# Kernel optimization log

Measured on AMD Instinct MI355X. Metric: run time of the kernel, lower is better.

Reference implementation:

```python
import jax, jax.numpy as jnp
import numpy as np

DIM, HEADS, DHEAD, CTX_DIM = 1024, 16, 64, 768
INNER = HEADS * DHEAD  # 1024
FF_HID = 4 * DIM       # 4096
EPS = 1e-5


def _ln(x, g, b):
    mu = jnp.mean(x, axis=-1, keepdims=True)
    var = jnp.mean(jnp.square(x - mu), axis=-1, keepdims=True)
    return (x - mu) * jax.lax.rsqrt(var + EPS) * g + b


def _attn(x, ctx, Wq, Wk, Wv, Wo, bo):
    b, n, _ = x.shape
    m = ctx.shape[1]
    q = (x @ Wq).reshape(b, n, HEADS, DHEAD)
    k = (ctx @ Wk).reshape(b, m, HEADS, DHEAD)
    v = (ctx @ Wv).reshape(b, m, HEADS, DHEAD)
    scale = DHEAD ** -0.5
    sim = jnp.einsum('bihd,bjhd->bhij', q, k) * scale
    attn = jax.nn.softmax(sim, axis=-1)
    out = jnp.einsum('bhij,bjhd->bihd', attn, v).reshape(b, n, INNER)
    return out @ Wo + bo


def setup_inputs() -> dict:
    key = jax.random.key(0)
    ks = jax.random.split(key, 24)
    def w(k, shape, fan_in):
        return jax.random.normal(k, shape, jnp.float32) * (fan_in ** -0.5)
    inp = {
        'x': jax.random.normal(ks[0], (2, 2048, DIM), jnp.float32),
        'context': jax.random.normal(ks[1], (2, 77, CTX_DIM), jnp.float32),
        # attn1 (self)
        'Wq1': w(ks[2], (DIM, INNER), DIM), 'Wk1': w(ks[3], (DIM, INNER), DIM),
        'Wv1': w(ks[4], (DIM, INNER), DIM), 'Wo1': w(ks[5], (INNER, DIM), INNER),
        'bo1': jnp.zeros((DIM,), jnp.float32),
        # attn2 (cross)
        'Wq2': w(ks[6], (DIM, INNER), DIM), 'Wk2': w(ks[7], (CTX_DIM, INNER), CTX_DIM),
        'Wv2': w(ks[8], (CTX_DIM, INNER), CTX_DIM), 'Wo2': w(ks[9], (INNER, DIM), INNER),
        'bo2': jnp.zeros((DIM,), jnp.float32),
        # GEGLU FFN
        'Wp': w(ks[10], (DIM, 2 * FF_HID), DIM), 'bp': jnp.zeros((2 * FF_HID,), jnp.float32),
        'W2': w(ks[11], (FF_HID, DIM), FF_HID), 'b2': jnp.zeros((DIM,), jnp.float32),
        # LayerNorms
        'g1': jnp.ones((DIM,), jnp.float32), 'be1': jnp.zeros((DIM,), jnp.float32),
        'g2': jnp.ones((DIM,), jnp.float32), 'be2': jnp.zeros((DIM,), jnp.float32),
        'g3': jnp.ones((DIM,), jnp.float32), 'be3': jnp.zeros((DIM,), jnp.float32),
    }
    return inp


def reference(x, context, Wq1, Wk1, Wv1, Wo1, bo1, Wq2, Wk2, Wv2, Wo2, bo2,
              Wp, bp, W2, b2, g1, be1, g2, be2, g3, be3):
    h = _ln(x, g1, be1)
    x = _attn(h, h, Wq1, Wk1, Wv1, Wo1, bo1) + x
    h = _ln(x, g2, be2)
    x = _attn(h, context, Wq2, Wk2, Wv2, Wo2, bo2) + x
    h = _ln(x, g3, be3)
    y = h @ Wp + bp
    a, gate = y[..., :FF_HID], y[..., FF_HID:]
    x = (a * jax.nn.gelu(gate, approximate=False)) @ W2 + b2 + x
    return x
```

## Files before the change

### kernel.cpp

```cpp
#include <hip/hip_runtime.h>
#include <hip/hip_bf16.h>
#include <math.h>

#define DIMN   1024
#define HEADS  16
#define DHEAD  64
#define CTXD   768
#define FFH    4096
#define NTOK   4096
#define SEQ    2048
#define NCTX   77
#define CTOK   154

typedef unsigned short u16;
typedef __bf16 bf16x8 __attribute__((ext_vector_type(8)));
typedef float  f32x4  __attribute__((ext_vector_type(4)));

__device__ __forceinline__ u16 f2bf(float f) {
  union { float f; unsigned u; } c; c.f = f;
  unsigned r = c.u + 0x7FFFu + ((c.u >> 16) & 1u);
  return (u16)(r >> 16);
}
__device__ __forceinline__ float bf2f(u16 h) {
  union { unsigned u; float f; } c; c.u = ((unsigned)h) << 16; return c.f;
}

__device__ __forceinline__ void gload16(const void* g, void* l) {
  __builtin_amdgcn_global_load_lds(
      (__attribute__((address_space(1))) void*)(void*)(g),
      (__attribute__((address_space(3))) void*)(l), 16, 0, 0);
}

__device__ __forceinline__ f32x4 mfma16(bf16x8 a, bf16x8 b, f32x4 c) {
  return __builtin_amdgcn_mfma_f32_16x16x32_bf16(a, b, c, 0, 0, 0);
}

struct WBatch { const float* s[6]; u16* d[6]; };

template<int NB>
__global__ __launch_bounds__(256)
void wconvB_k(WBatch wb, int K, int N)
{
  __shared__ u16 t[64][65];
  const float* __restrict__ W  = wb.s[blockIdx.z];
  u16* __restrict__       WT   = wb.d[blockIdx.z];
  int n0 = blockIdx.x * 64, k0 = blockIdx.y * 64;
  int tid = threadIdx.x;
  int rr = tid >> 4, cc = tid & 15;
#pragma unroll
  for (int i = 0; i < 4; ++i) {
    int kr = rr + i * 16;
    const float4 v = *(const float4*)&W[(size_t)(k0 + kr) * N + n0 + cc * 4];
    t[kr][cc*4+0] = f2bf(v.x); t[kr][cc*4+1] = f2bf(v.y);
    t[kr][cc*4+2] = f2bf(v.z); t[kr][cc*4+3] = f2bf(v.w);
  }
  __syncthreads();
#pragma unroll
  for (int i = 0; i < 4; ++i) {
    int nr = rr + i * 16;
    int r0 = cc * 4;
    ushort4 o;
    o.x = t[r0+0][nr]; o.y = t[r0+1][nr]; o.z = t[r0+2][nr]; o.w = t[r0+3][nr];
    *(ushort4*)&WT[(size_t)(n0 + nr) * K + k0 + r0] = o;
  }
}

__global__ __launch_bounds__(256)
void wconv_k(const float* __restrict__ W, u16* __restrict__ WT, int K, int N)
{
  __shared__ u16 t[64][65];
  int n0 = blockIdx.x * 64, k0 = blockIdx.y * 64;
  int tid = threadIdx.x;
  int rr = tid >> 4, cc = tid & 15;
#pragma unroll
  for (int i = 0; i < 4; ++i) {
    int kr = rr + i * 16;
    const float4 v = *(const float4*)&W[(size_t)(k0 + kr) * N + n0 + cc * 4];
    t[kr][cc*4+0] = f2bf(v.x); t[kr][cc*4+1] = f2bf(v.y);
    t[kr][cc*4+2] = f2bf(v.z); t[kr][cc*4+3] = f2bf(v.w);
  }
  __syncthreads();
#pragma unroll
  for (int i = 0; i < 4; ++i) {
    int nr = rr + i * 16;
    int r0 = cc * 4;
    ushort4 o;
    o.x = t[r0+0][nr]; o.y = t[r0+1][nr]; o.z = t[r0+2][nr]; o.w = t[r0+3][nr];
    *(ushort4*)&WT[(size_t)(n0 + nr) * K + k0 + r0] = o;
  }
}

__global__ void cconv_k(const float* __restrict__ c, u16* __restrict__ o, int n)
{
  int i = blockIdx.x * 256 + threadIdx.x;
  if (i < n) o[i] = f2bf(c[i]);
}

__global__ __launch_bounds__(256)
void ln_k(const float* __restrict__ x, const float* __restrict__ gm,
          const float* __restrict__ bt, u16* __restrict__ o)
{
  int row = blockIdx.x;
  int tid = threadIdx.x;
  const float4 v = *(const float4*)&x[(size_t)row * DIMN + tid * 4];
  float s = v.x + v.y + v.z + v.w;
  float q = v.x*v.x + v.y*v.y + v.z*v.z + v.w*v.w;
#pragma unroll
  for (int off = 32; off; off >>= 1) { s += __shfl_xor(s, off); q += __shfl_xor(q, off); }
  __shared__ float ss[4], qq[4];
  int wave = tid >> 6;
  if ((tid & 63) == 0) { ss[wave] = s; qq[wave] = q; }
  __syncthreads();
  s = ss[0] + ss[1] + ss[2] + ss[3];
  q = qq[0] + qq[1] + qq[2] + qq[3];
  float mu = s * (1.0f / DIMN);
  float var = q * (1.0f / DIMN) - mu * mu;
  float rs = rsqrtf(var + 1e-5f);
  const float4 gv = *(const float4*)&gm[tid * 4];
  const float4 bv = *(const float4*)&bt[tid * 4];
  ushort4 r;
  r.x = f2bf((v.x - mu) * rs * gv.x + bv.x);
  r.y = f2bf((v.y - mu) * rs * gv.y + bv.y);
  r.z = f2bf((v.z - mu) * rs * gv.z + bv.z);
  r.w = f2bf((v.w - mu) * rs * gv.w + bv.w);
  *(ushort4*)&o[(size_t)row * DIMN + tid * 4] = r;
}

__global__ __launch_bounds__(256)
void ln_b_k(const u16* __restrict__ x, const float* __restrict__ gm,
            const float* __restrict__ bt, u16* __restrict__ o)
{
  int row = blockIdx.x;
  int tid = threadIdx.x;
  const ushort4 u = *(const ushort4*)&x[(size_t)row * DIMN + tid * 4];
  float4 v;
  v.x = bf2f(u.x); v.y = bf2f(u.y); v.z = bf2f(u.z); v.w = bf2f(u.w);
  float s = v.x + v.y + v.z + v.w;
  float q = v.x*v.x + v.y*v.y + v.z*v.z + v.w*v.w;
#pragma unroll
  for (int off = 32; off; off >>= 1) { s += __shfl_xor(s, off); q += __shfl_xor(q, off); }
  __shared__ float ss[4], qq[4];
  int wave = tid >> 6;
  if ((tid & 63) == 0) { ss[wave] = s; qq[wave] = q; }
  __syncthreads();
  s = ss[0] + ss[1] + ss[2] + ss[3];
  q = qq[0] + qq[1] + qq[2] + qq[3];
  float mu = s * (1.0f / DIMN);
  float var = q * (1.0f / DIMN) - mu * mu;
  float rs = rsqrtf(var + 1e-5f);
  const float4 gv = *(const float4*)&gm[tid * 4];
  const float4 bv = *(const float4*)&bt[tid * 4];
  ushort4 r;
  r.x = f2bf((v.x - mu) * rs * gv.x + bv.x);
  r.y = f2bf((v.y - mu) * rs * gv.y + bv.y);
  r.z = f2bf((v.z - mu) * rs * gv.z + bv.z);
  r.w = f2bf((v.w - mu) * rs * gv.w + bv.w);
  *(ushort4*)&o[(size_t)row * DIMN + tid * 4] = r;
}

template<int MODE>
__global__ __launch_bounds__(512, 4)
void gemm_k(const u16* __restrict__ A, const u16* __restrict__ Bt,
            int M, int N, int K,
            const float* __restrict__ bias, const float* __restrict__ resid,
            u16* __restrict__ obf, float* __restrict__ of32,
            int seq, int vstride,
            u16* __restrict__ ob2, u16* __restrict__ ob3)
{
  __shared__ __align__(16) u16 As[2][128 * 32];
  __shared__ __align__(16) u16 Bs[2][128 * 32];
  const int tid = threadIdx.x;
  const int lane = tid & 63, wave = tid >> 6;
  const int wr = wave >> 1, wc = wave & 1;
  const int g = lane >> 4, r16 = lane & 15;
  const int m0 = blockIdx.x * 128, n0 = blockIdx.y * 128;

  f32x4 acc[2][4] = {};

  const int srow = tid >> 2;
  const int sch  = tid & 3;
  const int schs = sch ^ ((srow >> 1) & 3);
  const int arow = (m0 + srow > M - 1) ? (M - 1) : (m0 + srow);
  const size_t abase = (size_t)arow * K + schs * 8;
  const size_t bbase = (size_t)(n0 + srow) * K + schs * 8;

  auto stage = [&](int buf, int kt) {
    gload16(A  + abase + kt, &As[buf][tid * 8]);
    gload16(Bt + bbase + kt, &Bs[buf][tid * 8]);
  };

  stage(0, 0);

  const int nkt = K >> 5;
  for (int t = 0; t < nkt; ++t) {
    const int cur = t & 1;
    if (t + 1 < nkt) {
      stage(cur ^ 1, (t + 1) << 5);
      asm volatile("s_waitcnt vmcnt(2)" ::: "memory");
    } else {
      asm volatile("s_waitcnt vmcnt(0)" ::: "memory");
    }
    __builtin_amdgcn_s_barrier();

    bf16x8 af[2], bfr[4];
#pragma unroll
    for (int mi = 0; mi < 2; ++mi) {
      int r = wr * 32 + mi * 16 + r16;
      int cph = g ^ ((r >> 1) & 3);
      af[mi] = *(const bf16x8*)&As[cur][(r * 4 + cph) * 8];
    }
#pragma unroll
    for (int ni = 0; ni < 4; ++ni) {
      int r = wc * 64 + ni * 16 + r16;
      int cph = g ^ ((r >> 1) & 3);
      bfr[ni] = *(const bf16x8*)&Bs[cur][(r * 4 + cph) * 8];
    }
    __builtin_amdgcn_s_setprio(1);
#pragma unroll
    for (int mi = 0; mi < 2; ++mi)
#pragma unroll
      for (int ni = 0; ni < 4; ++ni)
        acc[mi][ni] = mfma16(af[mi], bfr[ni], acc[mi][ni]);
    __builtin_amdgcn_s_setprio(0);

    __builtin_amdgcn_s_barrier();
  }

  const int grp = n0 >> 10;
#pragma unroll
  for (int ni = 0; ni < 4; ++ni) {
    int col = n0 + wc * 64 + ni * 16 + r16;
    float bv = 0.0f;
    if constexpr (MODE == 0) bv = bias ? bias[col] : 0.0f;
    const int c1 = col & 1023;
#pragma unroll
    for (int mi = 0; mi < 2; ++mi) {
      f32x4 c = acc[mi][ni];
#pragma unroll
      for (int rg = 0; rg < 4; ++rg) {
        int row = m0 + wr * 32 + mi * 16 + g * 4 + rg;
        if (row < M) {
          float v = c[rg] + bv;
          if constexpr (MODE == 0) {
            obf[(size_t)row * N + col] = f2bf(v);
          } else if constexpr (MODE == 4) {
            if (grp == 0) {
              obf[(size_t)row * 1024 + c1] = f2bf(v);
            } else if (grp == 1) {
              ob2[(size_t)row * 1024 + c1] = f2bf(v);
            } else {
              int b = row / seq, srow_ = row - b * seq;
              int jg = srow_ >> 6, j = srow_ & 63;
              int pos = jg * 64 + ((j & 15) << 2) + (j >> 4);
              ob3[((size_t)b * HEADS * DHEAD + c1) * vstride + pos] = f2bf(v);
            }
          } else {
            if (grp == 0) {
              obf[(size_t)row * 1024 + c1] = f2bf(v);
            } else {
              int b = row / seq, srow_ = row - b * seq;
              int jg = srow_ >> 6, j = srow_ & 63;
              int pos = jg * 64 + ((j & 15) << 2) + (j >> 4);
              ob3[((size_t)b * HEADS * DHEAD + c1) * vstride + pos] = f2bf(v);
            }
          }
        }
      }
    }
  }
}

template<int MODE>
__global__ __launch_bounds__(512, 2)
void gemm64_k(const u16* __restrict__ A, const u16* __restrict__ Bt,
              int M, int N, int K,
              const float* __restrict__ bias, const float* __restrict__ residf,
              const u16* __restrict__ residb,
              u16* __restrict__ obf, float* __restrict__ of32)
{
  __shared__ __align__(16) u16 As[2][128 * 64];
  __shared__ __align__(16) u16 Bs[2][128 * 64];
  const int tid = threadIdx.x;
  const int lane = tid & 63, wave = tid >> 6;
  const int wr = wave >> 1, wc = wave & 1;
  const int g = lane >> 4, r16 = lane & 15;
  const int m0 = blockIdx.x * 128, n0 = blockIdx.y * 128;

  f32x4 acc[2][4] = {};

  int aro[2], bro[2], scs[2];
#pragma unroll
  for (int i = 0; i < 2; ++i) {
    const int c = tid + i * 512;
    const int r = c >> 3, ch = c & 7;
    scs[i] = ch ^ (r & 7);
    aro[i] = (m0 + r > M - 1) ? (M - 1) : (m0 + r);
    bro[i] = n0 + r;
  }

  auto stage = [&](int buf, int kt) {
#pragma unroll
    for (int i = 0; i < 2; ++i) {
      const int c = tid + i * 512;
      gload16(A  + (size_t)aro[i] * K + kt + scs[i] * 8, &As[buf][c * 8]);
      gload16(Bt + (size_t)bro[i] * K + kt + scs[i] * 8, &Bs[buf][c * 8]);
    }
  };

  stage(0, 0);

  const int nkt = K >> 6;
  for (int t = 0; t < nkt; ++t) {
    const int cur = t & 1;
    if (t + 1 < nkt) {
      stage(cur ^ 1, (t + 1) << 6);
      asm volatile("s_waitcnt vmcnt(4)" ::: "memory");
    } else {
      asm volatile("s_waitcnt vmcnt(0)" ::: "memory");
    }
    __builtin_amdgcn_s_barrier();

#pragma unroll
    for (int ks = 0; ks < 2; ++ks) {
      bf16x8 af[2], bfr[4];
#pragma unroll
      for (int mi = 0; mi < 2; ++mi) {
        int r = wr * 32 + mi * 16 + r16;
        int cph = (ks * 4 + g) ^ (r & 7);
        af[mi] = *(const bf16x8*)&As[cur][(r * 8 + cph) * 8];
      }
#pragma unroll
      for (int ni = 0; ni < 4; ++ni) {
        int r = wc * 64 + ni * 16 + r16;
        int cph = (ks * 4 + g) ^ (r & 7);
        bfr[ni] = *(const bf16x8*)&Bs[cur][(r * 8 + cph) * 8];
      }
      __builtin_amdgcn_s_setprio(1);
#pragma unroll
      for (int mi = 0; mi < 2; ++mi)
#pragma unroll
        for (int ni = 0; ni < 4; ++ni)
          acc[mi][ni] = mfma16(af[mi], bfr[ni], acc[mi][ni]);
      __builtin_amdgcn_s_setprio(0);
    }

    __builtin_amdgcn_s_barrier();
  }

#pragma unroll
  for (int ni = 0; ni < 4; ++ni) {
    int col = n0 + wc * 64 + ni * 16 + r16;
    float bv = bias ? bias[col] : 0.0f;
#pragma unroll
    for (int mi = 0; mi < 2; ++mi) {
      f32x4 c = acc[mi][ni];
#pragma unroll
      for (int rg = 0; rg < 4; ++rg) {
        int row = m0 + wr * 32 + mi * 16 + g * 4 + rg;
        if (row < M) {
          float v = c[rg] + bv;
          size_t o = (size_t)row * N + col;
          if constexpr (MODE == 0) {
            obf[o] = f2bf(v);
          } else if constexpr (MODE == 6) {
            obf[o] = f2bf(v + residf[o]);
          } else if constexpr (MODE == 7) {
            obf[o] = f2bf(v + bf2f(residb[o]));
          } else {
            of32[o] = v + bf2f(residb[o]);
          }
        }
      }
    }
  }
}

__global__ __launch_bounds__(512, 2)
void geglu_k(const u16* __restrict__ A, const u16* __restrict__ B1t,
             const u16* __restrict__ B2t,
             const float* __restrict__ ba, const float* __restrict__ bg,
             u16* __restrict__ out, int M, int N)
{
  __shared__ __align__(16) u16 As[2][128 * 32];
  __shared__ __align__(16) u16 B1s[2][128 * 32];
  __shared__ __align__(16) u16 B2s[2][128 * 32];
  const int tid = threadIdx.x;
  const int lane = tid & 63, wave = tid >> 6;
  const int wr = wave >> 1, wc = wave & 1;
  const int g = lane >> 4, r16 = lane & 15;
  const int m0 = blockIdx.x * 128, n0 = blockIdx.y * 128;
  const int K = 1024;

  f32x4 acca[2][4] = {}, accg[2][4] = {};

  const int srow = tid >> 2;
  const int sch  = tid & 3;
  const int schs = sch ^ ((srow >> 1) & 3);
  const size_t abase = (size_t)(m0 + srow) * K + schs * 8;
  const size_t bbase = (size_t)(n0 + srow) * K + schs * 8;

  auto stage = [&](int buf, int kt) {
    gload16(A   + abase + kt, &As[buf][tid * 8]);
    gload16(B1t + bbase + kt, &B1s[buf][tid * 8]);
    gload16(B2t + bbase + kt, &B2s[buf][tid * 8]);
  };

  stage(0, 0);

  const int nkt = K >> 5;
  for (int t = 0; t < nkt; ++t) {
    const int cur = t & 1;
    if (t + 1 < nkt) {
      stage(cur ^ 1, (t + 1) << 5);
      asm volatile("s_waitcnt vmcnt(3)" ::: "memory");
    } else {
      asm volatile("s_waitcnt vmcnt(0)" ::: "memory");
    }
    __builtin_amdgcn_s_barrier();

    bf16x8 af[2], b1f[4], b2f[4];
#pragma unroll
    for (int mi = 0; mi < 2; ++mi) {
      int r = wr * 32 + mi * 16 + r16;
      int cph = g ^ ((r >> 1) & 3);
      af[mi] = *(const bf16x8*)&As[cur][(r * 4 + cph) * 8];
    }
#pragma unroll
    for (int ni = 0; ni < 4; ++ni) {
      int r = wc * 64 + ni * 16 + r16;
      int cph = g ^ ((r >> 1) & 3);
      b1f[ni] = *(const bf16x8*)&B1s[cur][(r * 4 + cph) * 8];
      b2f[ni] = *(const bf16x8*)&B2s[cur][(r * 4 + cph) * 8];
    }
    __builtin_amdgcn_s_setprio(1);
#pragma unroll
    for (int mi = 0; mi < 2; ++mi)
#pragma unroll
      for (int ni = 0; ni < 4; ++ni) {
        acca[mi][ni] = mfma16(af[mi], b1f[ni], acca[mi][ni]);
        accg[mi][ni] = mfma16(af[mi], b2f[ni], accg[mi][ni]);
      }
    __builtin_amdgcn_s_setprio(0);

    __builtin_amdgcn_s_barrier();
  }

#pragma unroll
  for (int ni = 0; ni < 4; ++ni) {
    int col = n0 + wc * 64 + ni * 16 + r16;
    float bva = ba[col], bvg = bg[col];
#pragma unroll
    for (int mi = 0; mi < 2; ++mi) {
#pragma unroll
      for (int rg = 0; rg < 4; ++rg) {
        int row = m0 + wr * 32 + mi * 16 + g * 4 + rg;
        float a  = acca[mi][ni][rg] + bva;
        float gt = accg[mi][ni][rg] + bvg;
        float gl = 0.5f * gt * (1.0f + erff(gt * 0.70710678f));
        out[(size_t)row * N + col] = f2bf(a * gl);
      }
    }
  }
}

__global__ __launch_bounds__(256)
void attn_k(const u16* __restrict__ q, const u16* __restrict__ k,
            const u16* __restrict__ vt, u16* __restrict__ o,
            int kvlen, int seqk, int vstride)
{
  __shared__ __align__(16) u16 Ks[2][64 * 64];
  __shared__ __align__(16) u16 Vs[2][64 * 64];
  __shared__ __align__(16) u16 Ps[4][32 * 72];
  const int tid = threadIdx.x, lane = tid & 63, wave = tid >> 6;
  const int g = lane >> 4, r16 = lane & 15;

  const int L  = blockIdx.y * 16 + blockIdx.x;
  const int c8 = L & 7, tt = L >> 3;
  const int bx = tt & 15;
  const int bh = c8 + 8 * (tt >> 4);

  const int b = bh >> 4, h = bh & 15;
  const int q0 = bx * 128 + wave * 32;
  const float C = 0.18033688f;

  bf16x8 aq[2][2];
#pragma unroll
  for (int qs = 0; qs < 2; ++qs) {
    const size_t qoff = (size_t)(b * SEQ + q0 + qs * 16 + r16) * DIMN + h * DHEAD;
#pragma unroll
    for (int kc = 0; kc < 2; ++kc)
      aq[qs][kc] = *(const bf16x8*)&q[qoff + kc * 32 + g * 8];
  }
  asm volatile("" :: "v"(aq[0][0]), "v"(aq[0][1]), "v"(aq[1][0]), "v"(aq[1][1]));

  f32x4 oacc[2][4] = {};
  float mi[2][4], li[2][4];
#pragma unroll
  for (int qs = 0; qs < 2; ++qs)
#pragma unroll
    for (int rg = 0; rg < 4; ++rg) { mi[qs][rg] = -3e38f; li[qs][rg] = 0.f; }

  const size_t vtbase = (size_t)(b * HEADS + h) * DHEAD * vstride;
  const size_t kbase  = (size_t)b * seqk * DIMN + h * DHEAD;
  const int nkv = (kvlen + 63) >> 6;

  auto stage = [&](int buf, int kv0) {
#pragma unroll
    for (int i = 0; i < 2; ++i) {
      const int c = tid + i * 256;
      const int row = c >> 3, ch = c & 7;
      const int chs = ch ^ (row & 7);
      int kr = kv0 + row; if (kr > kvlen - 1) kr = kvlen - 1;
      gload16(k + kbase + (size_t)kr * DIMN + chs * 8, &Ks[buf][c * 8]);
    }
#pragma unroll
    for (int i = 0; i < 2; ++i) {
      const int c = tid + i * 256;
      const int row = c >> 3, ch = c & 7;
      const int chs = ch ^ (row & 7);
      gload16(vt + vtbase + (size_t)row * vstride + kv0 + chs * 8, &Vs[buf][c * 8]);
    }
  };

  stage(0, 0);

  for (int kvb = 0; kvb < nkv; ++kvb) {
    const int kv0 = kvb * 64;
    const int cur = kvb & 1;
    if (kvb + 1 < nkv) {
      stage(cur ^ 1, kv0 + 64);
      asm volatile("s_waitcnt vmcnt(4)" ::: "memory");
    } else {
      asm volatile("s_waitcnt vmcnt(0)" ::: "memory");
    }
    __builtin_amdgcn_s_barrier();

    f32x4 sa[2][4];
#pragma unroll
    for (int qs = 0; qs < 2; ++qs)
#pragma unroll
      for (int st = 0; st < 4; ++st) sa[qs][st] = (f32x4){0.f, 0.f, 0.f, 0.f};
    __builtin_amdgcn_s_setprio(1);
#pragma unroll
    for (int st = 0; st < 4; ++st) {
      const int kvr = st * 16 + r16;
#pragma unroll
      for (int kc = 0; kc < 2; ++kc) {
        const int chs = (kc * 4 + g) ^ (kvr & 7);
        const bf16x8 kf = *(const bf16x8*)&Ks[cur][kvr * 64 + chs * 8];
        sa[0][st] = mfma16(aq[0][kc], kf, sa[0][st]);
        sa[1][st] = mfma16(aq[1][kc], kf, sa[1][st]);
      }
    }
    __builtin_amdgcn_s_setprio(0);

    if (kv0 + 64 > kvlen) {
#pragma unroll
      for (int st = 0; st < 4; ++st)
        if (kv0 + st * 16 + r16 >= kvlen) {
#pragma unroll
          for (int qs = 0; qs < 2; ++qs)
#pragma unroll
            for (int rg = 0; rg < 4; ++rg) sa[qs][st][rg] = -3e38f;
        }
    }

    float bad = 0.f;
    float m4v[2][4];
#pragma unroll
    for (int qs = 0; qs < 2; ++qs)
#pragma unroll
      for (int rg = 0; rg < 4; ++rg) {
        float m4 = fmaxf(fmaxf(sa[qs][0][rg], sa[qs][1][rg]),
                         fmaxf(sa[qs][2][rg], sa[qs][3][rg]));
        m4v[qs][rg] = m4;
        bad = fmaxf(bad, m4 - mi[qs][rg]);
      }
    if (__any(bad > 16.0f)) {
#pragma unroll
      for (int qs = 0; qs < 2; ++qs)
#pragma unroll
        for (int rg = 0; rg < 4; ++rg) {
          float mx = m4v[qs][rg];
#pragma unroll
          for (int off = 1; off < 16; off <<= 1) mx = fmaxf(mx, __shfl_xor(mx, off));
          const float nm = fmaxf(mi[qs][rg], mx);
          const float corr = __builtin_amdgcn_exp2f((mi[qs][rg] - nm) * C);
          mi[qs][rg] = nm;
          li[qs][rg] *= corr;
#pragma unroll
          for (int ds = 0; ds < 4; ++ds) oacc[qs][ds][rg] *= corr;
        }
    }

#pragma unroll
    for (int qs = 0; qs < 2; ++qs) {
#pragma unroll
      for (int rg = 0; rg < 4; ++rg) {
        const float mc = mi[qs][rg] * C;
        const float p0 = __builtin_amdgcn_exp2f(__builtin_fmaf(sa[qs][0][rg], C, -mc));
        const float p1 = __builtin_amdgcn_exp2f(__builtin_fmaf(sa[qs][1][rg], C, -mc));
        const float p2 = __builtin_amdgcn_exp2f(__builtin_fmaf(sa[qs][2][rg], C, -mc));
        const float p3 = __builtin_amdgcn_exp2f(__builtin_fmaf(sa[qs][3][rg], C, -mc));
        li[qs][rg] += (p0 + p1) + (p2 + p3);
        unsigned lo, hi;
        asm("v_cvt_pk_bf16_f32 %0, %1, %2" : "=v"(lo) : "v"(p0), "v"(p1));
        asm("v_cvt_pk_bf16_f32 %0, %1, %2" : "=v"(hi) : "v"(p2), "v"(p3));
        const int prow = qs * 16 + g * 4 + rg;
        uint2 pk; pk.x = lo; pk.y = hi;
        *(uint2*)&Ps[wave][prow * 72 + r16 * 4] = pk;
      }
    }

    __builtin_amdgcn_s_setprio(1);
#pragma unroll
    for (int kc = 0; kc < 2; ++kc) {
      const bf16x8 pa0 = *(const bf16x8*)&Ps[wave][(r16)      * 72 + kc * 32 + g * 8];
      const bf16x8 pa1 = *(const bf16x8*)&Ps[wave][(16 + r16) * 72 + kc * 32 + g * 8];
#pragma unroll
      for (int ds = 0; ds < 4; ++ds) {
        const int dr = ds * 16 + r16;
        const int chs = (kc * 4 + g) ^ (dr & 7);
        const bf16x8 vf = *(const bf16x8*)&Vs[cur][dr * 64 + chs * 8];
        oacc[0][ds] = mfma16(pa0, vf, oacc[0][ds]);
        oacc[1][ds] = mfma16(pa1, vf, oacc[1][ds]);
      }
    }
    __builtin_amdgcn_s_setprio(0);

    __builtin_amdgcn_s_barrier();
  }

#pragma unroll
  for (int qs = 0; qs < 2; ++qs)
#pragma unroll
    for (int rg = 0; rg < 4; ++rg) {
      float s = li[qs][rg];
#pragma unroll
      for (int off = 1; off < 16; off <<= 1) s += __shfl_xor(s, off);
      li[qs][rg] = s;
    }

#pragma unroll
  for (int qs = 0; qs < 2; ++qs)
#pragma unroll
    for (int rg = 0; rg < 4; ++rg) {
      const float inv = 1.0f / li[qs][rg];
      const int row = q0 + qs * 16 + g * 4 + rg;
      const size_t base = (size_t)(b * SEQ + row) * DIMN + h * DHEAD;
#pragma unroll
      for (int ds = 0; ds < 4; ++ds)
        o[base + ds * 16 + r16] = f2bf(oacc[qs][ds][rg] * inv);
    }
}

extern "C" void kernel_launch(void* const* d_in, const int* in_sizes, int n_in,
                              void* d_out, int out_size, void* d_ws, size_t ws_size,
                              hipStream_t stream)
{
  const float* x   = (const float*)d_in[0];
  const float* ctx = (const float*)d_in[1];
  const float* Wq1 = (const float*)d_in[2];
  const float* Wk1 = (const float*)d_in[3];
  const float* Wv1 = (const float*)d_in[4];
  const float* Wo1 = (const float*)d_in[5];
  const float* bo1 = (const float*)d_in[6];
  const float* Wq2 = (const float*)d_in[7];
  const float* Wk2 = (const float*)d_in[8];
  const float* Wv2 = (const float*)d_in[9];
  const float* Wo2 = (const float*)d_in[10];
  const float* bo2 = (const float*)d_in[11];
  const float* Wp  = (const float*)d_in[12];
  const float* bp  = (const float*)d_in[13];
  const float* W2  = (const float*)d_in[14];
  const float* b2  = (const float*)d_in[15];
  const float* g1  = (const float*)d_in[16];
  const float* be1 = (const float*)d_in[17];
  const float* g2  = (const float*)d_in[18];
  const float* be2 = (const float*)d_in[19];
  const float* g3  = (const float*)d_in[20];
  const float* be3 = (const float*)d_in[21];

  char* ws = (char*)d_ws;
  size_t off = 0;
  auto alloc = [&](size_t bytes) -> void* {
    void* p = ws + off;
    off += (bytes + 255) & ~(size_t)255;
    return p;
  };

  u16* WqT1 = (u16*)alloc((size_t)1024 * 1024 * 2);
  u16* WkT1 = (u16*)alloc((size_t)1024 * 1024 * 2);
  u16* WvT1 = (u16*)alloc((size_t)1024 * 1024 * 2);
  u16* WoT1 = (u16*)alloc((size_t)1024 * 1024 * 2);
  u16* WqT2 = (u16*)alloc((size_t)1024 * 1024 * 2);
  u16* WkT2 = (u16*)alloc((size_t)1024 * 768 * 2);
  u16* WvT2 = (u16*)alloc((size_t)1024 * 768 * 2);
  u16* WoT2 = (u16*)alloc((size_t)1024 * 1024 * 2);
  u16* WpT  = (u16*)alloc((size_t)8192 * 1024 * 2);
  u16* W2T  = (u16*)alloc((size_t)1024 * 4096 * 2);
  u16* x1b  = (u16*)alloc((size_t)NTOK * DIMN * 2);
  u16* x2b  = (u16*)alloc((size_t)NTOK * DIMN * 2);
  u16* ctxb = (u16*)alloc((size_t)CTOK * CTXD * 2);
  u16* k2b  = (u16*)alloc((size_t)CTOK * DIMN * 2);
  u16* vt2b = (u16*)alloc((size_t)2 * HEADS * DHEAD * 128 * 2);
  u16* hb   = (u16*)alloc((size_t)NTOK * DIMN * 2);
  u16* qb   = (u16*)alloc((size_t)NTOK * DIMN * 2);
  u16* kb   = (u16*)alloc((size_t)NTOK * DIMN * 2);
  u16* vtb  = (u16*)alloc((size_t)NTOK * DIMN * 2);
  u16* ab   = (u16*)alloc((size_t)NTOK * DIMN * 2);
  u16* ub   = qb;

  dim3 blk(256);
  dim3 blk5(512);

  WBatch wb6;
  wb6.s[0] = Wq1; wb6.d[0] = WqT1;
  wb6.s[1] = Wk1; wb6.d[1] = WkT1;
  wb6.s[2] = Wv1; wb6.d[2] = WvT1;
  wb6.s[3] = Wo1; wb6.d[3] = WoT1;
  wb6.s[4] = Wq2; wb6.d[4] = WqT2;
  wb6.s[5] = Wo2; wb6.d[5] = WoT2;
  wconvB_k<6><<<dim3(16, 16, 6), blk, 0, stream>>>(wb6, 1024, 1024);
  WBatch wb2;
  wb2.s[0] = Wk2; wb2.d[0] = WkT2;
  wb2.s[1] = Wv2; wb2.d[1] = WvT2;
  wb2.s[2] = nullptr; wb2.d[2] = nullptr;
  wb2.s[3] = nullptr; wb2.d[3] = nullptr;
  wb2.s[4] = nullptr; wb2.d[4] = nullptr;
  wb2.s[5] = nullptr; wb2.d[5] = nullptr;
  wconvB_k<2><<<dim3(16, 12, 2), blk, 0, stream>>>(wb2, 768, 1024);
  wconv_k<<<dim3(128, 16), blk, 0, stream>>>(Wp, WpT, 1024, 8192);
  wconv_k<<<dim3(16, 64), blk, 0, stream>>>(W2, W2T, 4096, 1024);
  cconv_k<<<dim3((CTOK * CTXD + 255) / 256), blk, 0, stream>>>(ctx, ctxb, CTOK * CTXD);

  ln_k<<<NTOK, 256, 0, stream>>>(x, g1, be1, hb);
  gemm_k<4><<<dim3(32, 24), blk5, 0, stream>>>(hb, WqT1, NTOK, 3072, 1024, nullptr, nullptr, qb, nullptr, SEQ, SEQ, kb, vtb);
  attn_k<<<dim3(16, 32), blk, 0, stream>>>(qb, kb, vtb, ab, SEQ, SEQ, SEQ);
  gemm64_k<6><<<dim3(32, 8), blk5, 0, stream>>>(ab, WoT1, NTOK, 1024, 1024, bo1, x, nullptr, x1b, nullptr);

  ln_b_k<<<NTOK, 256, 0, stream>>>(x1b, g2, be2, hb);
  gemm64_k<0><<<dim3(32, 8), blk5, 0, stream>>>(hb, WqT2, NTOK, 1024, 1024, nullptr, nullptr, nullptr, qb, nullptr);
  gemm_k<5><<<dim3(2, 16), blk5, 0, stream>>>(ctxb, WkT2, CTOK, 2048, 768, nullptr, nullptr, k2b, nullptr, NCTX, 128, nullptr, vt2b);
  attn_k<<<dim3(16, 32), blk, 0, stream>>>(qb, k2b, vt2b, ab, NCTX, NCTX, 128);
  gemm64_k<7><<<dim3(32, 8), blk5, 0, stream>>>(ab, WoT2, NTOK, 1024, 1024, bo2, nullptr, x1b, x2b, nullptr);

  ln_b_k<<<NTOK, 256, 0, stream>>>(x2b, g3, be3, hb);
  geglu_k<<<dim3(32, 32), blk5, 0, stream>>>(hb, WpT, WpT + (size_t)4096 * 1024, bp, bp + 4096, ub, NTOK, FFH);
  gemm64_k<8><<<dim3(32, 8), blk5, 0, stream>>>(ub, W2T, NTOK, 1024, 4096, b2, nullptr, x2b, nullptr, (float*)d_out);

  (void)in_sizes; (void)n_in; (void)out_size; (void)ws_size;
}
```

Measured before the change: 401.0 us.

## Enlarge attention tiles to 256 queries and 128-key blocks with 8 waves

Reworks the attention kernel to use 512-thread blocks covering 256 query rows, with K/V staged in 128-key chunks instead of 64. The per-block LDS tiles, swizzle pattern for V (16-chunk XOR) and P buffer stride are widened to match, and the softmax/PV loops are extended to 8 score subtiles. The aim is to halve the number of KV iterations and barriers per block and share each staged K/V tile across more query rows. The cost is higher register and LDS use per block, which limits it to one block per CU. For cross-attention (77 keys), most of each 128-key tile is masked padding.

```diff
diff --git a/kernel.cpp b/kernel.cpp
--- a/kernel.cpp
+++ b/kernel.cpp
@@ -463,24 +463,24 @@
   }
 }
 
-__global__ __launch_bounds__(256)
+__global__ __launch_bounds__(512, 1)
 void attn_k(const u16* __restrict__ q, const u16* __restrict__ k,
             const u16* __restrict__ vt, u16* __restrict__ o,
             int kvlen, int seqk, int vstride)
 {
-  __shared__ __align__(16) u16 Ks[2][64 * 64];
-  __shared__ __align__(16) u16 Vs[2][64 * 64];
-  __shared__ __align__(16) u16 Ps[4][32 * 72];
+  __shared__ __align__(16) u16 Ks[2][128 * 64];
+  __shared__ __align__(16) u16 Vs[2][64 * 128];
+  __shared__ __align__(16) u16 Ps[8][32 * 136];
   const int tid = threadIdx.x, lane = tid & 63, wave = tid >> 6;
   const int g = lane >> 4, r16 = lane & 15;
 
-  const int L  = blockIdx.y * 16 + blockIdx.x;
+  const int L  = blockIdx.y * 8 + blockIdx.x;
   const int c8 = L & 7, tt = L >> 3;
-  const int bx = tt & 15;
-  const int bh = c8 + 8 * (tt >> 4);
+  const int bx = tt & 7;
+  const int bh = c8 * 4 + (tt >> 3);
 
   const int b = bh >> 4, h = bh & 15;
-  const int q0 = bx * 128 + wave * 32;
+  const int q0 = bx * 256 + wave * 32;
   const float C = 0.18033688f;
 
   bf16x8 aq[2][2];
@@ -502,12 +502,12 @@
 
   const size_t vtbase = (size_t)(b * HEADS + h) * DHEAD * vstride;
   const size_t kbase  = (size_t)b * seqk * DIMN + h * DHEAD;
-  const int nkv = (kvlen + 63) >> 6;
+  const int nkv = (kvlen + 127) >> 7;
 
   auto stage = [&](int buf, int kv0) {
 #pragma unroll
     for (int i = 0; i < 2; ++i) {
-      const int c = tid + i * 256;
+      const int c = tid + i * 512;
       const int row = c >> 3, ch = c & 7;
       const int chs = ch ^ (row & 7);
       int kr = kv0 + row; if (kr > kvlen - 1) kr = kvlen - 1;
@@ -515,9 +515,9 @@
     }
 #pragma unroll
     for (int i = 0; i < 2; ++i) {
-      const int c = tid + i * 256;
-      const int row = c >> 3, ch = c & 7;
-      const int chs = ch ^ (row & 7);
+      const int c = tid + i * 512;
+      const int row = c >> 4, ch = c & 15;
+      const int chs = ch ^ (row & 15);
       gload16(vt + vtbase + (size_t)row * vstride + kv0 + chs * 8, &Vs[buf][c * 8]);
     }
   };
@@ -525,24 +525,24 @@
   stage(0, 0);
 
   for (int kvb = 0; kvb < nkv; ++kvb) {
-    const int kv0 = kvb * 64;
+    const int kv0 = kvb * 128;
     const int cur = kvb & 1;
     if (kvb + 1 < nkv) {
-      stage(cur ^ 1, kv0 + 64);
+      stage(cur ^ 1, kv0 + 128);
       asm volatile("s_waitcnt vmcnt(4)" ::: "memory");
     } else {
       asm volatile("s_waitcnt vmcnt(0)" ::: "memory");
     }
     __builtin_amdgcn_s_barrier();
 
-    f32x4 sa[2][4];
+    f32x4 sa[2][8];
 #pragma unroll
     for (int qs = 0; qs < 2; ++qs)
 #pragma unroll
-      for (int st = 0; st < 4; ++st) sa[qs][st] = (f32x4){0.f, 0.f, 0.f, 0.f};
+      for (int st = 0; st < 8; ++st) sa[qs][st] = (f32x4){0.f, 0.f, 0.f, 0.f};
     __builtin_amdgcn_s_setprio(1);
 #pragma unroll
-    for (int st = 0; st < 4; ++st) {
+    for (int st = 0; st < 8; ++st) {
       const int kvr = st * 16 + r16;
 #pragma unroll
       for (int kc = 0; kc < 2; ++kc) {
@@ -554,9 +554,9 @@
     }
     __builtin_amdgcn_s_setprio(0);
 
-    if (kv0 + 64 > kvlen) {
-#pragma unroll
-      for (int st = 0; st < 4; ++st)
+    if (kv0 + 128 > kvlen) {
+#pragma unroll
+      for (int st = 0; st < 8; ++st)
         if (kv0 + st * 16 + r16 >= kvlen) {
 #pragma unroll
           for (int qs = 0; qs < 2; ++qs)
@@ -573,6 +573,8 @@
       for (int rg = 0; rg < 4; ++rg) {
         float m4 = fmaxf(fmaxf(sa[qs][0][rg], sa[qs][1][rg]),
                          fmaxf(sa[qs][2][rg], sa[qs][3][rg]));
+        m4 = fmaxf(m4, fmaxf(fmaxf(sa[qs][4][rg], sa[qs][5][rg]),
+                             fmaxf(sa[qs][6][rg], sa[qs][7][rg])));
         m4v[qs][rg] = m4;
         bad = fmaxf(bad, m4 - mi[qs][rg]);
       }
@@ -598,30 +600,35 @@
 #pragma unroll
       for (int rg = 0; rg < 4; ++rg) {
         const float mc = mi[qs][rg] * C;
-        const float p0 = __builtin_amdgcn_exp2f(__builtin_fmaf(sa[qs][0][rg], C, -mc));
-        const float p1 = __builtin_amdgcn_exp2f(__builtin_fmaf(sa[qs][1][rg], C, -mc));
-        const float p2 = __builtin_amdgcn_exp2f(__builtin_fmaf(sa[qs][2][rg], C, -mc));
-        const float p3 = __builtin_amdgcn_exp2f(__builtin_fmaf(sa[qs][3][rg], C, -mc));
-        li[qs][rg] += (p0 + p1) + (p2 + p3);
-        unsigned lo, hi;
-        asm("v_cvt_pk_bf16_f32 %0, %1, %2" : "=v"(lo) : "v"(p0), "v"(p1));
-        asm("v_cvt_pk_bf16_f32 %0, %1, %2" : "=v"(hi) : "v"(p2), "v"(p3));
+        float p[8];
+#pragma unroll
+        for (int st = 0; st < 8; ++st)
+          p[st] = __builtin_amdgcn_exp2f(__builtin_fmaf(sa[qs][st][rg], C, -mc));
+        li[qs][rg] += ((p[0] + p[1]) + (p[2] + p[3])) + ((p[4] + p[5]) + (p[6] + p[7]));
+        unsigned w0, w1, w2, w3;
+        asm("v_cvt_pk_bf16_f32 %0, %1, %2" : "=v"(w0) : "v"(p[0]), "v"(p[1]));
+        asm("v_cvt_pk_bf16_f32 %0, %1, %2" : "=v"(w1) : "v"(p[2]), "v"(p[3]));
+        asm("v_cvt_pk_bf16_f32 %0, %1, %2" : "=v"(w2) : "v"(p[4]), "v"(p[5]));
+        asm("v_cvt_pk_bf16_f32 %0, %1, %2" : "=v"(w3) : "v"(p[6]), "v"(p[7]));
         const int prow = qs * 16 + g * 4 + rg;
-        uint2 pk; pk.x = lo; pk.y = hi;
-        *(uint2*)&Ps[wave][prow * 72 + r16 * 4] = pk;
+        uint2 pk0; pk0.x = w0; pk0.y = w1;
+        uint2 pk1; pk1.x = w2; pk1.y = w3;
+        *(uint2*)&Ps[wave][prow * 136 + r16 * 4]      = pk0;
+        *(uint2*)&Ps[wave][prow * 136 + 64 + r16 * 4] = pk1;
       }
     }
 
     __builtin_amdgcn_s_setprio(1);
 #pragma unroll
-    for (int kc = 0; kc < 2; ++kc) {
-      const bf16x8 pa0 = *(const bf16x8*)&Ps[wave][(r16)      * 72 + kc * 32 + g * 8];
-      const bf16x8 pa1 = *(const bf16x8*)&Ps[wave][(16 + r16) * 72 + kc * 32 + g * 8];
+    for (int kc = 0; kc < 4; ++kc) {
+      const bf16x8 pa0 = *(const bf16x8*)&Ps[wave][(r16)      * 136 + kc * 32 + g * 8];
+      const bf16x8 pa1 = *(const bf16x8*)&Ps[wave][(16 + r16) * 136 + kc * 32 + g * 8];
 #pragma unroll
       for (int ds = 0; ds < 4; ++ds) {
         const int dr = ds * 16 + r16;
-        const int chs = (kc * 4 + g) ^ (dr & 7);
-        const bf16x8 vf = *(const bf16x8*)&Vs[cur][dr * 64 + chs * 8];
+        const int cc = kc * 4 + g;
+        const int chs = cc ^ (dr & 15);
+        const bf16x8 vf = *(const bf16x8*)&Vs[cur][dr * 128 + chs * 8];
         oacc[0][ds] = mfma16(pa0, vf, oacc[0][ds]);
         oacc[1][ds] = mfma16(pa1, vf, oacc[1][ds]);
       }
@@ -736,13 +743,13 @@
 
   ln_k<<<NTOK, 256, 0, stream>>>(x, g1, be1, hb);
   gemm_k<4><<<dim3(32, 24), blk5, 0, stream>>>(hb, WqT1, NTOK, 3072, 1024, nullptr, nullptr, qb, nullptr, SEQ, SEQ, kb, vtb);
-  attn_k<<<dim3(16, 32), blk, 0, stream>>>(qb, kb, vtb, ab, SEQ, SEQ, SEQ);
+  attn_k<<<dim3(8, 32), blk5, 0, stream>>>(qb, kb, vtb, ab, SEQ, SEQ, SEQ);
   gemm64_k<6><<<dim3(32, 8), blk5, 0, stream>>>(ab, WoT1, NTOK, 1024, 1024, bo1, x, nullptr, x1b, nullptr);
 
   ln_b_k<<<NTOK, 256, 0, stream>>>(x1b, g2, be2, hb);
   gemm64_k<0><<<dim3(32, 8), blk5, 0, stream>>>(hb, WqT2, NTOK, 1024, 1024, nullptr, nullptr, nullptr, qb, nullptr);
   gemm_k<5><<<dim3(2, 16), blk5, 0, stream>>>(ctxb, WkT2, CTOK, 2048, 768, nullptr, nullptr, k2b, nullptr, NCTX, 128, nullptr, vt2b);
-  attn_k<<<dim3(16, 32), blk, 0, stream>>>(qb, k2b, vt2b, ab, NCTX, NCTX, 128);
+  attn_k<<<dim3(8, 32), blk5, 0, stream>>>(qb, k2b, vt2b, ab, NCTX, NCTX, 128);
   gemm64_k<7><<<dim3(32, 8), blk5, 0, stream>>>(ab, WoT2, NTOK, 1024, 1024, bo2, nullptr, x1b, x2b, nullptr);
 
   ln_b_k<<<NTOK, 256, 0, stream>>>(x2b, g3, be3, hb);
```

New measurement: 390.0 us. 1.03x faster.
